# Kernel optimization log

Hardware: AMD Instinct MI355X
Metric: run time of the kernel (lower is better)

## Reference

```python
import jax, jax.numpy as jnp
import numpy as np

LOG2PI = float(np.log(2.0 * np.pi))


def setup_inputs() -> dict:
    key = jax.random.key(0)
    k1, k2, k3 = jax.random.split(key, 3)
    batch, dim_z, n_samples = 1024, 32, 32
    mean = jax.random.normal(k1, (batch, dim_z), dtype=jnp.float32)
    logvar = jax.random.normal(k2, (batch, dim_z), dtype=jnp.float32)
    eps = jax.random.normal(k3, (batch, n_samples, dim_z), dtype=jnp.float32)
    return {"mean": mean, "logvar": logvar, "eps": eps,
            "n_samples": n_samples, "agg_size": 256}


def reference(mean, logvar, eps, n_samples, agg_size):
    batch, dim_z = mean.shape
    if batch % agg_size != 0:
        agg_size = batch
    nc = batch // agg_size  # num_chunks
    # GaussianReParameterize: z ~ N(mean, exp(logvar)), shape [B, n_samples, dim_z]
    std = jnp.exp(0.5 * logvar)
    z = mean[:, None, :] + eps * std[:, None, :]
    # z2: [nc, agg_size*n_samples, dim_z]
    z2 = z.reshape(nc, agg_size * n_samples, dim_z)
    # component params broadcast against all samples in the chunk
    mu = mean.reshape(nc, agg_size, 1, dim_z)
    lv = logvar.reshape(nc, agg_size, 1, dim_z)
    # per-dimension Gaussian log-PDF of each sample under each component:
    # [nc, agg_size, agg_size*n_samples, dim_z]
    log_q_ijk = -0.5 * ((z2[:, None, :, :] - mu) ** 2 * jnp.exp(-lv) + lv + LOG2PI)
    # mixture density per dimension: mean over components, then log, then mean over samples
    logq = jnp.log(jnp.exp(log_q_ijk).mean(axis=1)).mean(axis=1)  # [nc, dim_z]
    # log standard-normal density per dimension, averaged over samples
    logp = (-0.5 * (z2 ** 2 + LOG2PI)).mean(axis=1)  # [nc, dim_z]
    okl = (logq - logp).mean(axis=0)  # [dim_z]
    return okl.sum(axis=-1)
```

## Files before the change

### kernel.cpp

```cpp
#include <hip/hip_runtime.h>
#include <math.h>

#define B    1024
#define D    32
#define AGG  256
#define NC   4
#define M    8192
#define NEV  1024

#define TN     1024
#define ZMIN   (-32.0f)
#define INVH   16.0f
#define HH     0.0625f
#define ZCLAMP 31.8f

#define WS_PARAMS  8192
#define WS_MSDT    532480
#define WS_TABLE   794624
#define WS_EPST    1318912
#define WS_NEED    5513216

#define LOG2E 1.4426950408889634f
#define LN2   0.6931471805599453f

__global__ __launch_bounds__(256) void kprep(const float* __restrict__ eps,
                                             const float* __restrict__ mean,
                                             const float* __restrict__ logvar,
                                             float* __restrict__ epsT,
                                             float4* __restrict__ params,
                                             float2* __restrict__ msdT)
{
    const int bid = blockIdx.x;
    const int t   = threadIdx.x;

    {
        const int c   = bid >> 8;
        const int j0t = (bid & 255) << 5;
        const int x   = t & 31;
        const int y0  = t >> 5;
        __shared__ float tile[32][33];
#pragma unroll
        for (int p = 0; p < 4; ++p) {
            const int r = (p << 3) + y0;
            tile[r][x] = eps[((size_t)c * M + j0t + r) * D + x];
        }
        __syncthreads();
#pragma unroll
        for (int p = 0; p < 4; ++p) {
            const int kk = (p << 3) + y0;
            epsT[(((size_t)c * D + kk) << 13) + j0t + x] = tile[x][kk];
        }
    }

    if (bid < 128) {
        const int tid = bid * 256 + t;
        const int row = tid >> 5;
        const int k   = tid & (D - 1);
        const int c   = row >> 8;
        const int i   = row & (AGG - 1);
        const int ck  = (c << 5) | k;
        const float mu = mean[tid];
        const float lv = logvar[tid];
        const float ev = __builtin_amdgcn_exp2f(-lv * LOG2E);
        const float A  = -0.5f * LOG2E * ev;
        params[(ck << 8) | i] =
            make_float4(A, LOG2E * mu * ev,
                        -0.5f * LOG2E * fmaf(mu * mu, ev, lv),
                        __builtin_amdgcn_exp2f(A * 0.0078125f));
        msdT[(ck << 8) | i] = make_float2(mu, __builtin_amdgcn_exp2f(0.5f * LOG2E * lv));
    }
}

__global__ __launch_bounds__(1024) void ktable(const float4* __restrict__ params,
                                               float* __restrict__ table)
{
    const int bid  = blockIdx.x;
    const int ck   = bid >> 1;
    const int seg  = bid & 1;
    const int t    = threadIdx.x;
    const int lane = t & 63;
    const int wv   = t >> 6;

    __shared__ float4 ps[AGG];
    if (t < AGG) ps[t] = params[(ck << 8) | t];
    __syncthreads();

    const int g0   = (seg << 9) + (lane << 3);
    const float z0 = fmaf((float)g0, HH, ZMIN);
    const float tz = z0 + z0 + HH;
    float a0 = 0.f, a1 = 0.f, a2 = 0.f, a3 = 0.f;
    float a4 = 0.f, a5 = 0.f, a6 = 0.f, a7 = 0.f;
#pragma unroll
    for (int i = 0; i < 16; ++i) {
        const float4 p = ps[(wv << 4) + i];
        const float ap = fmaf(p.x, z0, p.y);
        float w = __builtin_amdgcn_exp2f(fmaf(ap, z0, p.z));
        float d = HH * fmaf(p.x, tz, p.y);
        d = fminf(d, 126.f);
        float r = __builtin_amdgcn_exp2f(d);
        a0 += w;
        w *= r; a1 += w; r *= p.w;
        w *= r; a2 += w; r *= p.w;
        w *= r; a3 += w; r *= p.w;
        w *= r; a4 += w; r *= p.w;
        w *= r; a5 += w; r *= p.w;
        w *= r; a6 += w; r *= p.w;
        w *= r; a7 += w;
    }

    __shared__ float part[16][512];
    {
        float* pb = &part[wv][lane << 3];
        *(float4*)pb       = make_float4(a0, a1, a2, a3);
        *(float4*)(pb + 4) = make_float4(a4, a5, a6, a7);
    }
    __syncthreads();
    if (t < 512) {
        float s = 0.f;
#pragma unroll
        for (int w = 0; w < 16; ++w) s += part[w][t];
        table[(ck << 10) | (seg << 9) | t] =
            __builtin_amdgcn_logf(fmaxf(s, 1e-30f));
    }
}

__global__ __launch_bounds__(256) void keval(const float* __restrict__ epsT,
                                             const float2* __restrict__ msdT,
                                             const float* __restrict__ table,
                                             float* __restrict__ partial)
{
    const int bid = blockIdx.x;
    const int ck  = bid >> 3;
    const int q   = bid & 7;
    const int j0  = q << 10;
    const int t   = threadIdx.x;

    const float4 e4 = *(const float4*)(epsT + ((size_t)ck << 13) + j0 + (t << 2));
    const float e[4] = {e4.x, e4.y, e4.z, e4.w};

    __shared__ float2 rowp[32];
    if (t < 32) rowp[t] = msdT[(ck << 8) + (q << 5) + t];

    __shared__ float tab[TN];
    const float* __restrict__ gt = table + (ck << 10);
#pragma unroll
    for (int p = 0; p < 4; ++p)
        tab[t + (p << 8)] = gt[t + (p << 8)];
    __syncthreads();

    const float2 ms = rowp[t >> 3];
    float r = 0.f;
#pragma unroll
    for (int u = 0; u < 4; ++u) {
        const float z  = fmaf(e[u], ms.y, ms.x);
        const float zc = fminf(fmaxf(z, -ZCLAMP), ZCLAMP);
        const float x  = fmaf(zc, INVH, 512.0f);
        const float fg = floorf(x);
        const float f  = x - fg;
        const int  ig  = (int)fg;
        const float Lm = tab[ig - 1];
        const float L0 = tab[ig];
        const float L1 = tab[ig + 1];
        const float L2 = tab[ig + 2];
        const float m0 = 0.5f * (L1 - Lm);
        const float m1 = 0.5f * (L2 - L0);
        const float dl = L1 - L0;
        const float c2 = 3.f * dl - 2.f * m0 - m1;
        const float c3 = m0 + m1 - 2.f * dl;
        const float L  = fmaf(f, fmaf(f, fmaf(f, c3, c2), m0), L0);
        r += fmaf(LN2, L, 0.5f * z * z);
    }

    for (int off = 32; off > 0; off >>= 1) r += __shfl_down(r, off, 64);
    __shared__ float wsum[4];
    if ((t & 63) == 0) wsum[t >> 6] = r;
    __syncthreads();
    if (t == 0) partial[bid] = (wsum[0] + wsum[1]) + (wsum[2] + wsum[3]);
}

__global__ __launch_bounds__(256) void kfinal(const float* __restrict__ partial,
                                              float* __restrict__ out)
{
    const int t = threadIdx.x;
    double s = 0.0;
#pragma unroll
    for (int i = 0; i < NEV / 256; ++i) s += (double)partial[i * 256 + t];
    __shared__ double sd[256];
    sd[t] = s;
    __syncthreads();
    for (int off = 128; off > 0; off >>= 1) {
        if (t < off) sd[t] += sd[t + off];
        __syncthreads();
    }
    if (t == 0)
        out[0] = (float)(sd[0] * (1.0 / (double)(NC * M))
                         - (double)D * 5.545177444479562);
}

__global__ __launch_bounds__(256) void kfb(const float* __restrict__ eps,
                                           const float* __restrict__ mean,
                                           const float* __restrict__ logvar,
                                           float* __restrict__ partial)
{
    const int bid = blockIdx.x;
    const int ck  = bid >> 3;
    const int q   = bid & 7;
    const int c   = ck >> 5;
    const int k   = ck & (D - 1);
    const int j0  = q << 10;
    const int t   = threadIdx.x;

    __shared__ float4 prm[AGG];
    {
        const int row  = (c << 8) + t;
        const float mu = mean[row * D + k];
        const float lv = logvar[row * D + k];
        const float ev = __builtin_amdgcn_exp2f(-lv * LOG2E);
        prm[t] = make_float4(-0.5f * LOG2E * ev, LOG2E * mu * ev,
                             -0.5f * LOG2E * fmaf(mu * mu, ev, lv),
                             __builtin_amdgcn_exp2f(0.5f * LOG2E * lv));
    }
    __syncthreads();

    float zv[4], acc[4];
#pragma unroll
    for (int u = 0; u < 4; ++u) {
        const int j    = j0 + t + (u << 8);
        const float4 p = prm[j >> 5];
        const float mu = -0.5f * p.y * __builtin_amdgcn_rcpf(p.x);
        zv[u]  = fmaf(eps[(size_t)((c << 13) + j) * D + k], p.w, mu);
        acc[u] = 0.f;
    }
#pragma unroll 4
    for (int i = 0; i < AGG; ++i) {
        const float4 p = prm[i];
#pragma unroll
        for (int u = 0; u < 4; ++u)
            acc[u] += __builtin_amdgcn_exp2f(fmaf(fmaf(p.x, zv[u], p.y), zv[u], p.z));
    }
    float r = 0.f;
#pragma unroll
    for (int u = 0; u < 4; ++u)
        r += LN2 * __builtin_amdgcn_logf(acc[u]) + 0.5f * zv[u] * zv[u];

    for (int off = 32; off > 0; off >>= 1) r += __shfl_down(r, off, 64);
    __shared__ float wsum[4];
    if ((t & 63) == 0) wsum[t >> 6] = r;
    __syncthreads();
    if (t == 0) partial[bid] = (wsum[0] + wsum[1]) + (wsum[2] + wsum[3]);
}

extern "C" void kernel_launch(void* const* d_in, const int* in_sizes, int n_in,
                              void* d_out, int out_size, void* d_ws, size_t ws_size,
                              hipStream_t stream)
{
    const float* mean   = (const float*)d_in[0];
    const float* logvar = (const float*)d_in[1];
    const float* eps    = (const float*)d_in[2];
    float* out = (float*)d_out;

    float*  partial = (float*)d_ws;
    float4* params  = (float4*)((char*)d_ws + WS_PARAMS);
    float2* msdT    = (float2*)((char*)d_ws + WS_MSDT);
    float*  table   = (float*)((char*)d_ws + WS_TABLE);
    float*  epsT    = (float*)((char*)d_ws + WS_EPST);

    if (ws_size >= (size_t)WS_NEED) {
        kprep<<<NC * 256, 256, 0, stream>>>(eps, mean, logvar, epsT, params, msdT);
        ktable<<<256, 1024, 0, stream>>>(params, table);
        keval<<<NEV, 256, 0, stream>>>(epsT, msdT, table, partial);
    } else {
        kfb<<<NEV, 256, 0, stream>>>(eps, mean, logvar, partial);
    }
    kfinal<<<1, 256, 0, stream>>>(partial, out);
}
```

Baseline: 21.34 us.

## Drop prep kernel; compute params inline and store table derivatives for Hermite lookup

Removes the separate kprep kernel that transposed eps and precomputed per-component parameters. Those parameters are now computed inside the table kernel, which also accumulates the analytic derivative of the mixture log-density and stores (log, slope) pairs. The eval kernel reads eps in its natural layout, computes std on the fly, and interpolates from the global table with two float2 loads instead of staging four-point stencils in shared memory. This saves one launch and the eps transpose round-trip, at the cost of extra accumulators in the table kernel and uncached, scattered global table reads in eval.

```diff
diff --git a/kernel.cpp b/kernel.cpp
--- a/kernel.cpp
+++ b/kernel.cpp
@@ -12,67 +12,17 @@
 #define ZMIN   (-32.0f)
 #define INVH   16.0f
 #define HH     0.0625f
-#define ZCLAMP 31.8f
-
-#define WS_PARAMS  8192
-#define WS_MSDT    532480
-#define WS_TABLE   794624
-#define WS_EPST    1318912
-#define WS_NEED    5513216
+#define ZCLAMP 31.9f
+
+#define WS_TABLE 8192
+#define WS_NEED  (8192 + 128 * TN * 8)
 
 #define LOG2E 1.4426950408889634f
 #define LN2   0.6931471805599453f
 
-__global__ __launch_bounds__(256) void kprep(const float* __restrict__ eps,
-                                             const float* __restrict__ mean,
-                                             const float* __restrict__ logvar,
-                                             float* __restrict__ epsT,
-                                             float4* __restrict__ params,
-                                             float2* __restrict__ msdT)
-{
-    const int bid = blockIdx.x;
-    const int t   = threadIdx.x;
-
-    {
-        const int c   = bid >> 8;
-        const int j0t = (bid & 255) << 5;
-        const int x   = t & 31;
-        const int y0  = t >> 5;
-        __shared__ float tile[32][33];
-#pragma unroll
-        for (int p = 0; p < 4; ++p) {
-            const int r = (p << 3) + y0;
-            tile[r][x] = eps[((size_t)c * M + j0t + r) * D + x];
-        }
-        __syncthreads();
-#pragma unroll
-        for (int p = 0; p < 4; ++p) {
-            const int kk = (p << 3) + y0;
-            epsT[(((size_t)c * D + kk) << 13) + j0t + x] = tile[x][kk];
-        }
-    }
-
-    if (bid < 128) {
-        const int tid = bid * 256 + t;
-        const int row = tid >> 5;
-        const int k   = tid & (D - 1);
-        const int c   = row >> 8;
-        const int i   = row & (AGG - 1);
-        const int ck  = (c << 5) | k;
-        const float mu = mean[tid];
-        const float lv = logvar[tid];
-        const float ev = __builtin_amdgcn_exp2f(-lv * LOG2E);
-        const float A  = -0.5f * LOG2E * ev;
-        params[(ck << 8) | i] =
-            make_float4(A, LOG2E * mu * ev,
-                        -0.5f * LOG2E * fmaf(mu * mu, ev, lv),
-                        __builtin_amdgcn_exp2f(A * 0.0078125f));
-        msdT[(ck << 8) | i] = make_float2(mu, __builtin_amdgcn_exp2f(0.5f * LOG2E * lv));
-    }
-}
-
-__global__ __launch_bounds__(1024) void ktable(const float4* __restrict__ params,
-                                               float* __restrict__ table)
+__global__ __launch_bounds__(1024) void ktable2(const float* __restrict__ mean,
+                                                const float* __restrict__ logvar,
+                                                float2* __restrict__ table)
 {
     const int bid  = blockIdx.x;
     const int ck   = bid >> 1;
@@ -82,7 +32,18 @@
     const int wv   = t >> 6;
 
     __shared__ float4 ps[AGG];
-    if (t < AGG) ps[t] = params[(ck << 8) | t];
+    if (t < AGG) {
+        const int c   = ck >> 5;
+        const int k   = ck & (D - 1);
+        const int row = (c << 8) + t;
+        const float mu = mean[row * D + k];
+        const float lv = logvar[row * D + k];
+        const float ev = __builtin_amdgcn_exp2f(-lv * LOG2E);
+        const float A  = -0.5f * LOG2E * ev;
+        ps[t] = make_float4(A, LOG2E * mu * ev,
+                            -0.5f * LOG2E * fmaf(mu * mu, ev, lv),
+                            __builtin_amdgcn_exp2f(A * 0.0078125f));
+    }
     __syncthreads();
 
     const int g0   = (seg << 9) + (lane << 3);
@@ -90,84 +51,90 @@
     const float tz = z0 + z0 + HH;
     float a0 = 0.f, a1 = 0.f, a2 = 0.f, a3 = 0.f;
     float a4 = 0.f, a5 = 0.f, a6 = 0.f, a7 = 0.f;
+    float d0 = 0.f, d1 = 0.f, d2 = 0.f, d3 = 0.f;
+    float d4 = 0.f, d5 = 0.f, d6 = 0.f, d7 = 0.f;
 #pragma unroll
     for (int i = 0; i < 16; ++i) {
         const float4 p = ps[(wv << 4) + i];
         const float ap = fmaf(p.x, z0, p.y);
         float w = __builtin_amdgcn_exp2f(fmaf(ap, z0, p.z));
-        float d = HH * fmaf(p.x, tz, p.y);
-        d = fminf(d, 126.f);
-        float r = __builtin_amdgcn_exp2f(d);
-        a0 += w;
-        w *= r; a1 += w; r *= p.w;
-        w *= r; a2 += w; r *= p.w;
-        w *= r; a3 += w; r *= p.w;
-        w *= r; a4 += w; r *= p.w;
-        w *= r; a5 += w; r *= p.w;
-        w *= r; a6 += w; r *= p.w;
-        w *= r; a7 += w;
-    }
-
-    __shared__ float part[16][512];
+        float dd = HH * fmaf(p.x, tz, p.y);
+        dd = fminf(dd, 126.f);
+        float r = __builtin_amdgcn_exp2f(dd);
+        const float qd = p.x * 0.125f;
+        float q = fmaf(p.x, z0, ap);
+        a0 += w; d0 = fmaf(w, q, d0); q += qd;
+        w *= r; a1 += w; d1 = fmaf(w, q, d1); q += qd; r *= p.w;
+        w *= r; a2 += w; d2 = fmaf(w, q, d2); q += qd; r *= p.w;
+        w *= r; a3 += w; d3 = fmaf(w, q, d3); q += qd; r *= p.w;
+        w *= r; a4 += w; d4 = fmaf(w, q, d4); q += qd; r *= p.w;
+        w *= r; a5 += w; d5 = fmaf(w, q, d5); q += qd; r *= p.w;
+        w *= r; a6 += w; d6 = fmaf(w, q, d6); q += qd; r *= p.w;
+        w *= r; a7 += w; d7 = fmaf(w, q, d7);
+    }
+
+    __shared__ float2 part[16][512];
     {
-        float* pb = &part[wv][lane << 3];
-        *(float4*)pb       = make_float4(a0, a1, a2, a3);
-        *(float4*)(pb + 4) = make_float4(a4, a5, a6, a7);
+        float2* pb = &part[wv][lane << 3];
+        pb[0] = make_float2(a0, d0); pb[1] = make_float2(a1, d1);
+        pb[2] = make_float2(a2, d2); pb[3] = make_float2(a3, d3);
+        pb[4] = make_float2(a4, d4); pb[5] = make_float2(a5, d5);
+        pb[6] = make_float2(a6, d6); pb[7] = make_float2(a7, d7);
     }
     __syncthreads();
     if (t < 512) {
-        float s = 0.f;
-#pragma unroll
-        for (int w = 0; w < 16; ++w) s += part[w][t];
+        float s = 0.f, d = 0.f;
+#pragma unroll
+        for (int w = 0; w < 16; ++w) {
+            const float2 pw = part[w][t];
+            s += pw.x; d += pw.y;
+        }
+        const float sg = fmaxf(s, 1e-30f);
         table[(ck << 10) | (seg << 9) | t] =
-            __builtin_amdgcn_logf(fmaxf(s, 1e-30f));
-    }
-}
-
-__global__ __launch_bounds__(256) void keval(const float* __restrict__ epsT,
-                                             const float2* __restrict__ msdT,
-                                             const float* __restrict__ table,
-                                             float* __restrict__ partial)
-{
-    const int bid = blockIdx.x;
-    const int ck  = bid >> 3;
-    const int q   = bid & 7;
-    const int j0  = q << 10;
-    const int t   = threadIdx.x;
-
-    const float4 e4 = *(const float4*)(epsT + ((size_t)ck << 13) + j0 + (t << 2));
-    const float e[4] = {e4.x, e4.y, e4.z, e4.w};
-
-    __shared__ float2 rowp[32];
-    if (t < 32) rowp[t] = msdT[(ck << 8) + (q << 5) + t];
-
-    __shared__ float tab[TN];
-    const float* __restrict__ gt = table + (ck << 10);
-#pragma unroll
-    for (int p = 0; p < 4; ++p)
-        tab[t + (p << 8)] = gt[t + (p << 8)];
-    __syncthreads();
-
-    const float2 ms = rowp[t >> 3];
+            make_float2(__builtin_amdgcn_logf(sg),
+                        d * __builtin_amdgcn_rcpf(sg) * HH);
+    }
+}
+
+__global__ __launch_bounds__(256) void keval2(const float* __restrict__ eps,
+                                              const float* __restrict__ mean,
+                                              const float* __restrict__ logvar,
+                                              const float2* __restrict__ table,
+                                              float* __restrict__ partial)
+{
+    const int t    = threadIdx.x;
+    const int gidx = (blockIdx.x * 256 + t) << 2;
+    const int c    = gidx >> 18;
+    const int r18  = gidx & 262143;
+    const int j    = r18 >> 5;
+    const int k0   = r18 & 31;
+    const int row  = (c << 8) + (j >> 5);
+    const int ckb  = (c << 5) + k0;
+
+    const float4 e4 = *(const float4*)(eps + gidx);
+    const float4 m4 = *(const float4*)(mean + row * D + k0);
+    const float4 l4 = *(const float4*)(logvar + row * D + k0);
+    const float e[4]  = {e4.x, e4.y, e4.z, e4.w};
+    const float mu[4] = {m4.x, m4.y, m4.z, m4.w};
+    const float lv[4] = {l4.x, l4.y, l4.z, l4.w};
+
     float r = 0.f;
 #pragma unroll
-    for (int u = 0; u < 4; ++u) {
-        const float z  = fmaf(e[u], ms.y, ms.x);
+    for (int kk = 0; kk < 4; ++kk) {
+        const float sd = __builtin_amdgcn_exp2f(0.5f * LOG2E * lv[kk]);
+        const float z  = fmaf(e[kk], sd, mu[kk]);
         const float zc = fminf(fmaxf(z, -ZCLAMP), ZCLAMP);
         const float x  = fmaf(zc, INVH, 512.0f);
         const float fg = floorf(x);
         const float f  = x - fg;
         const int  ig  = (int)fg;
-        const float Lm = tab[ig - 1];
-        const float L0 = tab[ig];
-        const float L1 = tab[ig + 1];
-        const float L2 = tab[ig + 2];
-        const float m0 = 0.5f * (L1 - Lm);
-        const float m1 = 0.5f * (L2 - L0);
-        const float dl = L1 - L0;
-        const float c2 = 3.f * dl - 2.f * m0 - m1;
-        const float c3 = m0 + m1 - 2.f * dl;
-        const float L  = fmaf(f, fmaf(f, fmaf(f, c3, c2), m0), L0);
+        const float2* __restrict__ tg = table + ((ckb + kk) << 10);
+        const float2 n0 = tg[ig];
+        const float2 n1 = tg[ig + 1];
+        const float dl  = n1.x - n0.x;
+        const float c2  = 3.f * dl - 2.f * n0.y - n1.y;
+        const float c3  = n0.y + n1.y - 2.f * dl;
+        const float L   = fmaf(f, fmaf(f, fmaf(f, c3, c2), n0.y), n0.x);
         r += fmaf(LN2, L, 0.5f * z * z);
     }
 
@@ -175,7 +142,7 @@
     __shared__ float wsum[4];
     if ((t & 63) == 0) wsum[t >> 6] = r;
     __syncthreads();
-    if (t == 0) partial[bid] = (wsum[0] + wsum[1]) + (wsum[2] + wsum[3]);
+    if (t == 0) partial[blockIdx.x] = (wsum[0] + wsum[1]) + (wsum[2] + wsum[3]);
 }
 
 __global__ __launch_bounds__(256) void kfinal(const float* __restrict__ partial,
@@ -260,15 +227,11 @@
     float* out = (float*)d_out;
 
     float*  partial = (float*)d_ws;
-    float4* params  = (float4*)((char*)d_ws + WS_PARAMS);
-    float2* msdT    = (float2*)((char*)d_ws + WS_MSDT);
-    float*  table   = (float*)((char*)d_ws + WS_TABLE);
-    float*  epsT    = (float*)((char*)d_ws + WS_EPST);
+    float2* table   = (float2*)((char*)d_ws + WS_TABLE);
 
     if (ws_size >= (size_t)WS_NEED) {
-        kprep<<<NC * 256, 256, 0, stream>>>(eps, mean, logvar, epsT, params, msdT);
-        ktable<<<256, 1024, 0, stream>>>(params, table);
-        keval<<<NEV, 256, 0, stream>>>(epsT, msdT, table, partial);
+        ktable2<<<256, 1024, 0, stream>>>(mean, logvar, table);
+        keval2<<<NEV, 256, 0, stream>>>(eps, mean, logvar, table, partial);
     } else {
         kfb<<<NEV, 256, 0, stream>>>(eps, mean, logvar, partial);
     }
```

Measured after the change: 18.04 us. -15.5%, faster.
